# Kernel tuning notes

Hardware: AMD Instinct MI355X
Metric: run time of the kernel (lower is better)

The kernel has to match this reference:

```python
import jax, jax.numpy as jnp
import numpy as np

BIT = 64
N_CLASS = 100
NUM_TRAIN = 100000
BATCH = 512
MU = 1.0   # config['mu']
M = 1.0    # config['m']
ETA = 0.5  # config['eta']
VUL = 1.0  # config['vul']
NTA = 1.0  # config['nta']


def setup_inputs() -> dict:
    key = jax.random.key(0)
    k1, k2, k3, k4, k5, k6 = jax.random.split(key, 6)
    u = jax.random.normal(k1, (BATCH, BIT), jnp.float32)
    # y / Y are one-hot label matrices in DFH; build realistic one-hot floats
    labels = jax.random.randint(k2, (BATCH,), 0, N_CLASS)
    y = jax.nn.one_hot(labels, N_CLASS, dtype=jnp.float32)
    ind = jax.random.randint(k3, (BATCH,), 0, NUM_TRAIN)
    U = jax.random.normal(k4, (BIT, NUM_TRAIN), jnp.float32)
    train_labels = jax.random.randint(k5, (NUM_TRAIN,), 0, N_CLASS)
    Y = jax.nn.one_hot(train_labels, N_CLASS, dtype=jnp.float32).T  # [n_class, num_train]
    V = jax.random.normal(k6, (BIT, N_CLASS), jnp.float32)
    return {"u": u, "y": y, "ind": ind, "U": U, "Y": Y, "V": V}


def _center_gradient(V, y, b):
    # 200-step gradient descent on V minimizing intra + vul*inter + nta*quant.
    n_class = V.shape[1]
    TK = V.shape[0] * (2.0 * jnp.eye(n_class, dtype=V.dtype)
                       - jnp.ones((n_class, n_class), V.dtype))
    yt = y.T  # [n_class, batch]

    def inner_loss(Vc):
        intra = jnp.mean((Vc @ yt - b) ** 2)
        inter = jnp.mean((Vc.T @ Vc - TK) ** 2)
        quant = jnp.mean((Vc - jnp.sign(Vc)) ** 2)
        return intra + VUL * inter + NTA * quant

    grad_fn = jax.grad(inner_loss)

    def step(Vc, i):
        # torch code multiplies alpha by 0.1 *before* the update at i==149 and i==179
        alpha = 0.03 * jnp.where(i >= 149, 0.1, 1.0) * jnp.where(i >= 179, 0.1, 1.0)
        return Vc - alpha * grad_fn(Vc), None

    V_new, _ = jax.lax.scan(step, V, jnp.arange(200))
    return V_new


def reference(u, y, ind, U, Y, V):
    # state buffer updates (torch: self.U[:, ind] = u.t().data, etc.)
    U = U.at[:, ind].set(u.T)
    Y = Y.at[:, ind].set(y.T)
    C = jnp.sign(V)
    b = jnp.sign(MU * (C @ y.T) + u.T)                     # [bit, batch]
    V_new = _center_gradient(V, y, b)                      # updated self.V
    s = (y @ Y > 0).astype(u.dtype)                        # [batch, num_train]
    ip = jnp.clip(0.5 * (u @ U), -100.0, 50.0)             # [batch, num_train]
    metric_loss = jnp.mean((1.0 - s) * jnp.log1p(jnp.exp(M + ip))
                           + s * jnp.log1p(jnp.exp(M - ip)))
    quantization_loss = jnp.mean((b - u.T) ** 2)
    loss = metric_loss + ETA * quantization_loss
    return loss, V_new
```

## Files before the change

kernel.cpp:

```cpp
#include <hip/hip_runtime.h>

#define BIT 64
#define NCLASS 100
#define NTRAIN 100000
#define BATCH 512

#define O_OWNER   0
#define O_LAB     200000
#define O_BSUM    233280
#define O_COUNT   239680
#define O_QSUM    239780
#define O_MSUM    239782

typedef __attribute__((ext_vector_type(8))) short short8v;
typedef __attribute__((ext_vector_type(4))) float f32x4;
typedef unsigned short ushortT;

__device__ __forceinline__ float signf(float x) {
    return (x > 0.f) ? 1.f : ((x < 0.f) ? -1.f : 0.f);
}

__device__ __forceinline__ unsigned cvtpk(float lo, float hi) {
    unsigned r;
    asm("v_cvt_pk_bf16_f32 %0, %1, %2" : "=v"(r) : "v"(lo), "v"(hi));
    return r;
}
__device__ __forceinline__ float dpp_x1(float x) {
    union { float f; int i; } v; v.f = x;
    v.i = __builtin_amdgcn_mov_dpp(v.i, 0xB1, 0xF, 0xF, false);
    return v.f;
}
__device__ __forceinline__ float dpp_x2(float x) {
    union { float f; int i; } v; v.f = x;
    v.i = __builtin_amdgcn_mov_dpp(v.i, 0x4E, 0xF, 0xF, false);
    return v.f;
}

__global__ __launch_bounds__(512) void k_pre(
        const float* __restrict__ y, const int* __restrict__ ind,
        const float* __restrict__ u, const float* __restrict__ V,
        int* owner, int* lab, float* Bsum, float* count, double* qsum) {
    __shared__ float srow[BATCH];
    __shared__ int   labl[BATCH];
    __shared__ double wq[8];
    const int r = blockIdx.x;
    const int bb = threadIdx.x;

    const float* yrow = y + bb * NCLASS;
    int best = 0;
    for (int c = 0; c < NCLASS; ++c)
        if (yrow[c] > 0.5f) best = c;
    labl[bb] = best;
    if (r == 0) {
        lab[bb] = best;
        atomicMax(&owner[ind[bb]], bb);
    }

    const float v  = V[r * NCLASS + best];
    const float uu = u[bb * BIT + r];
    const float bv = signf(signf(v) + uu);
    srow[bb] = bv;
    const float d = bv - uu;
    double q = (double)(d * d);
    for (int off = 32; off; off >>= 1) q += __shfl_down(q, off);
    const int wid = bb >> 6, lane = bb & 63;
    if (lane == 0) wq[wid] = q;
    __syncthreads();
    if (bb == 0) {
        double s = 0;
        for (int w = 0; w < 8; ++w) s += wq[w];
        atomicAdd(qsum, s);
    }

    if (bb < NCLASS) {
        float s = 0.f; int n = 0;
        for (int k = 0; k < BATCH; ++k) {
            const bool hit = (labl[k] == bb);
            s += hit ? srow[k] : 0.f;
            n += hit;
        }
        Bsum[r * NCLASS + bb] = s;
        if (r == 0) count[bb] = (float)n;
    }
}

__global__ __launch_bounds__(512, 4) void k_main(
        const float* __restrict__ V, const float* __restrict__ Bsum,
        const float* __restrict__ count, const float* __restrict__ u,
        const float* __restrict__ U, const float* __restrict__ Y,
        const int* __restrict__ lab, const int* __restrict__ owner,
        double* msum, float* __restrict__ out) {
    __shared__ __align__(16) char smem[69888];

    if (blockIdx.x == 0) {
        ushortT* SAb = (ushortT*)smem;
        ushortT* SBb = (ushortT*)(smem + 32768);
        ushortT* SMf = (ushortT*)(smem + 61440);
        float*   rs  = (float*)(smem + 69632);

        const int t = threadIdx.x, l = t & 63, w = t >> 6;
        const int g = l >> 4, c16 = l & 15;
        const int h = w >> 2;
        const int mtile = w & 3;
        const int m = mtile * 16 + c16;
        const bool dg = ((mtile >> 1) == h);
        const short8v ONES = {0x3F80,0x3F80,0x3F80,0x3F80,
                              0x3F80,0x3F80,0x3F80,0x3F80};

        for (int i = t; i < 16384; i += 512) SAb[i] = 0;
        for (int i = t; i < 14336; i += 512) SBb[i] = 0;

        const float ci = 2.0f / 32768.0f;
        const float ce = 4.0f / 10000.0f;
        const float cq = 2.0f / 6400.0f;
        const float ce64 = 64.0f * ce;

        bool live[4];
        int sbO[4];
        float vreg[4][4], Kc[4][4], ncib[4][4];
        #pragma unroll
        for (int q = 0; q < 4; ++q) {
            const int nt = 4 * h + q;
            const int n0 = nt * 16 + 4 * g;
            const bool wact = (nt < 7);
            live[q] = wact && (n0 < NCLASS);
            sbO[q] = ((nt * 2 + (mtile >> 1)) * 64 +
                      (16 * (c16 >> 2) + 4 * g + (c16 & 3))) * 8 + 4 * (mtile & 1);
            #pragma unroll
            for (int r = 0; r < 4; ++r) {
                float v = 0.f, bs = 0.f, cn = 0.f;
                if (live[q]) {
                    const int n = n0 + r;
                    v  = V[m * NCLASS + n];
                    bs = Bsum[m * NCLASS + n];
                    cn = count[n];
                }
                vreg[q][r] = v;
                Kc[q][r]   = ci * cn + cq - 128.f * ce;
                ncib[q][r] = -ci * bs;
            }
        }
        const int saO0 = (mtile * 4 + 2 * h) * 512 + l * 8;
        const int saO1 = saO0 + 512;

        auto store_frags = [&](ushortT* SAn, ushortT* SBn) {
            uint4 wa;
            wa.x = cvtpk(vreg[0][0], vreg[0][1]);
            wa.y = cvtpk(vreg[0][2], vreg[0][3]);
            wa.z = cvtpk(vreg[1][0], vreg[1][1]);
            wa.w = cvtpk(vreg[1][2], vreg[1][3]);
            *(uint4*)&SAn[saO0] = wa;
            wa.x = cvtpk(vreg[2][0], vreg[2][1]);
            wa.y = cvtpk(vreg[2][2], vreg[2][3]);
            wa.z = cvtpk(vreg[3][0], vreg[3][1]);
            wa.w = cvtpk(vreg[3][2], vreg[3][3]);
            *(uint4*)&SAn[saO1] = wa;
            #pragma unroll
            for (int q = 0; q < 4; ++q) {
                if (4 * h + q < 7) {
                    float a0 = vreg[q][0], a1 = vreg[q][1];
                    float a2 = vreg[q][2], a3 = vreg[q][3];
                    float t0 = dpp_x1(a1), t1 = dpp_x1(a0);
                    float t2 = dpp_x1(a3), t3 = dpp_x1(a2);
                    const bool o1 = (l & 1);
                    float c0 = o1 ? t0 : a0;
                    float c1 = o1 ? a1 : t1;
                    float c2 = o1 ? t2 : a2;
                    float c3 = o1 ? a3 : t3;
                    float u0 = dpp_x2(c2), u1 = dpp_x2(c3);
                    float u2 = dpp_x2(c0), u3 = dpp_x2(c1);
                    const bool o2 = (l & 2);
                    float d0 = o2 ? u0 : c0;
                    float d1 = o2 ? u1 : c1;
                    float d2 = o2 ? c2 : u2;
                    float d3 = o2 ? c3 : u3;
                    uint2 wb;
                    wb.x = cvtpk(d0, d1);
                    wb.y = cvtpk(d2, d3);
                    *(uint2*)&SBn[sbO[q]] = wb;
                }
            }
        };

        __syncthreads();
        store_frags(SAb, SBb);
        __syncthreads();

        int cur = 0;
        for (int step = 0; step < 200; ++step) {
            float alpha = 0.03f;
            if (step >= 149) alpha *= 0.1f;
            if (step >= 179) alpha *= 0.1f;

            const ushortT* SAc = SAb + cur * 8192;

            f32x4 aM0 = {0.f,0.f,0.f,0.f}, aM1 = {0.f,0.f,0.f,0.f};
            f32x4 aR  = {0.f,0.f,0.f,0.f};
            #pragma unroll
            for (int ks = 0; ks < 4; ++ks) {
                short8v b  = *(const short8v*)&SAc[mtile * 2048 + ks * 512 + l * 8];
                short8v a0 = *(const short8v*)&SAc[(2 * h) * 2048 + ks * 512 + l * 8];
                short8v a1 = *(const short8v*)&SAc[(2 * h + 1) * 2048 + ks * 512 + l * 8];
                aM0 = __builtin_amdgcn_mfma_f32_16x16x32_bf16(a0, b, aM0, 0, 0, 0);
                aM1 = __builtin_amdgcn_mfma_f32_16x16x32_bf16(a1, b, aM1, 0, 0, 0);
                if (dg)
                    aR = __builtin_amdgcn_mfma_f32_16x16x32_bf16(b, ONES, aR, 0, 0, 0);
            }
            {
                uint4 sm;
                sm.x = cvtpk(aM0[0], aM0[1]);
                sm.y = cvtpk(aM0[2], aM0[3]);
                sm.z = cvtpk(aM1[0], aM1[1]);
                sm.w = cvtpk(aM1[2], aM1[3]);
                *(uint4*)&SMf[(mtile * 2 + h) * 512 + l * 8] = sm;
            }
            if (dg && c16 == 0)
                *(f32x4*)&rs[mtile * 16 + 4 * g] = aR;
            __syncthreads();

            const ushortT* SBc = SBb + cur * 7168;
            f32x4 p[4];
            #pragma unroll
            for (int q = 0; q < 4; ++q) p[q] = (f32x4){0.f,0.f,0.f,0.f};
            #pragma unroll
            for (int kb = 0; kb < 2; ++kb) {
                short8v bP = *(const short8v*)&SMf[(mtile * 2 + kb) * 512 + l * 8];
                #pragma unroll
                for (int q = 0; q < 4; ++q) {
                    if (4 * h + q < 7) {
                        short8v aP = *(const short8v*)
                            &SBc[((4 * h + q) * 2 + kb) * 512 + l * 8];
                        p[q] = __builtin_amdgcn_mfma_f32_16x16x32_bf16(aP, bP, p[q], 0, 0, 0);
                    }
                }
            }
            const float rsm = rs[m];

            #pragma unroll
            for (int q = 0; q < 4; ++q) {
                if (4 * h + q < 7) {
                    #pragma unroll
                    for (int r = 0; r < 4; ++r) {
                        const float v = vreg[q][r];
                        float t1 = __builtin_fmaf(Kc[q][r], v, ncib[q][r]);
                        t1 = __builtin_fmaf(ce,   p[q][r], t1);
                        t1 = __builtin_fmaf(ce64, rsm,     t1);
                        t1 -= __builtin_copysignf(cq, v);
                        float vn = __builtin_fmaf(-alpha, t1, v);
                        vreg[q][r] = live[q] ? vn : 0.f;
                    }
                }
            }
            store_frags(SAb + (cur ^ 1) * 8192, SBb + (cur ^ 1) * 7168);
            __syncthreads();
            cur ^= 1;
        }

        #pragma unroll
        for (int q = 0; q < 4; ++q) {
            if (live[q]) {
                const int n0 = (4 * h + q) * 16 + 4 * g;
                #pragma unroll
                for (int r = 0; r < 4; ++r)
                    out[1 + m * NCLASS + n0 + r] = vreg[q][r];
            }
        }
    } else {
        float*  ut   = (float*)smem;
        int*    slab = (int*)(smem + 34816);
        double* wsum = (double*)(smem + 36864);
        int*    tls  = (int*)(smem + 36928);

        const int t = threadIdx.x;
        const int jj = t & 255;
        const int j = (blockIdx.x - 1) * 256 + jj;
        const int half = t >> 8;
        const bool jok = (j < NTRAIN);
        slab[t] = lab[t];

        if (half == 0) {
            int tl = 0;
            if (jok) {
                for (int c = 0; c < NCLASS; ++c)
                    if (Y[(size_t)c * NTRAIN + j] > 0.5f) tl = c;
                int ow = owner[j];
                if (ow >= 0) tl = lab[ow];
            }
            tls[jj] = tl;
        }
        __syncthreads();
        const int tl = tls[jj];

        const float* colbase = U;
        size_t cstride = NTRAIN;
        if (jok) {
            int ow = owner[j];
            if (ow >= 0) { colbase = u + (size_t)ow * BIT; cstride = 1; }
            else         { colbase = U + j; }
        }

        float lsum = 0.f;
        for (int ch = 0; ch < 4; ++ch) {
            __syncthreads();
            for (int i = t; i < 8192; i += 512) {
                int buf = i >> 12, k = (i >> 6) & 63, r = i & 63;
                ut[buf * 4352 + r * 68 + k] = u[((buf * 4 + ch) * 64 + k) * BIT + r];
            }
            __syncthreads();

            if (jok) {
                const float* myut = ut + half * 4352;
                float acc[64];
                #pragma unroll
                for (int k = 0; k < 64; ++k) acc[k] = 0.f;
                #pragma unroll 2
                for (int r = 0; r < BIT; ++r) {
                    float Uv = colbase[(size_t)r * cstride];
                    const float* urow = &myut[r * 68];
                    #pragma unroll
                    for (int qq = 0; qq < 16; ++qq) {
                        float4 uv = *(const float4*)&urow[qq * 4];
                        acc[4 * qq + 0] += uv.x * Uv;
                        acc[4 * qq + 1] += uv.y * Uv;
                        acc[4 * qq + 2] += uv.z * Uv;
                        acc[4 * qq + 3] += uv.w * Uv;
                    }
                }
                const int b0 = (half * 4 + ch) * 64;
                #pragma unroll
                for (int k = 0; k < 64; ++k) {
                    float ip = fminf(fmaxf(0.5f * acc[k], -100.f), 50.f);
                    float x = (slab[b0 + k] == tl) ? (1.0f - ip) : (1.0f + ip);
                    lsum += fmaxf(x, 0.f) + __logf(1.f + __expf(-fabsf(x)));
                }
            }
        }

        double d = (double)lsum;
        for (int off = 32; off; off >>= 1) d += __shfl_down(d, off);
        const int wid = t >> 6, lane = t & 63;
        if (lane == 0) wsum[wid] = d;
        __syncthreads();
        if (t == 0) {
            double s = 0;
            for (int ww = 0; ww < 8; ++ww) s += wsum[ww];
            atomicAdd(msum, s);
        }
    }
}

__global__ void k_final(const double* __restrict__ msum,
                        const double* __restrict__ qsum, float* out) {
    if (threadIdx.x == 0) {
        double loss = (*msum) / ((double)BATCH * (double)NTRAIN)
                    + 0.5 * ((*qsum) / ((double)BIT * (double)BATCH));
        out[0] = (float)loss;
    }
}

extern "C" void kernel_launch(void* const* d_in, const int* in_sizes, int n_in,
                              void* d_out, int out_size, void* d_ws, size_t ws_size,
                              hipStream_t stream) {
    const float* u   = (const float*)d_in[0];
    const float* y   = (const float*)d_in[1];
    const int*   ind = (const int*)d_in[2];
    const float* U   = (const float*)d_in[3];
    const float* Y   = (const float*)d_in[4];
    const float* V   = (const float*)d_in[5];
    float* out = (float*)d_out;

    int*   wsI = (int*)d_ws;
    float* wsF = (float*)d_ws;
    int*   owner = wsI + O_OWNER;
    int*   lab   = wsI + O_LAB;
    float* Bsum  = wsF + O_BSUM;
    float* count = wsF + O_COUNT;
    double* qsum = (double*)(wsF + O_QSUM);
    double* msum = (double*)(wsF + O_MSUM);

    hipMemsetAsync(owner, 0xFF, NTRAIN * sizeof(int), stream);
    hipMemsetAsync(wsF + O_QSUM, 0, 4 * sizeof(float), stream);

    k_pre<<<64, 512, 0, stream>>>(y, ind, u, V, owner, lab, Bsum, count, qsum);
    k_main<<<1 + (NTRAIN + 255) / 256, 512, 0, stream>>>(
        V, Bsum, count, u, U, Y, lab, owner, msum, out);
    k_final<<<1, 64, 0, stream>>>(msum, qsum, out);
}
```

Baseline: 364.6 us.

## Precompute transposed u in global memory and split main kernel into noinline bodies

```diff
diff --git a/kernel.cpp b/kernel.cpp
--- a/kernel.cpp
+++ b/kernel.cpp
@@ -7,6 +7,7 @@
 
 #define O_OWNER   0
 #define O_LAB     200000
+#define O_UT      200512
 #define O_BSUM    233280
 #define O_COUNT   239680
 #define O_QSUM    239780
@@ -39,7 +40,8 @@
 __global__ __launch_bounds__(512) void k_pre(
         const float* __restrict__ y, const int* __restrict__ ind,
         const float* __restrict__ u, const float* __restrict__ V,
-        int* owner, int* lab, float* Bsum, float* count, double* qsum) {
+        int* owner, int* lab, float* Bsum, float* count, double* qsum,
+        float* uT) {
     __shared__ float srow[BATCH];
     __shared__ int   labl[BATCH];
     __shared__ double wq[8];
@@ -58,6 +60,7 @@
 
     const float v  = V[r * NCLASS + best];
     const float uu = u[bb * BIT + r];
+    uT[r * BATCH + bb] = uu;
     const float bv = signf(signf(v) + uu);
     srow[bb] = bv;
     const float d = bv - uu;
@@ -84,268 +87,274 @@
     }
 }
 
-__global__ __launch_bounds__(512, 4) void k_main(
+__device__ __noinline__ void gd_body(
+        const float* __restrict__ V, const float* __restrict__ Bsum,
+        const float* __restrict__ count, float* __restrict__ out) {
+    __shared__ ushortT SAb[16384];
+    __shared__ ushortT SBb[14336];
+    __shared__ ushortT SMf[4096];
+    __shared__ float   rs[64];
+    __shared__ float   xpad[4096];
+
+    const int t = threadIdx.x, l = t & 63, w = t >> 6;
+    ((volatile float*)xpad)[t] = 0.f;
+
+    const int g = l >> 4, c16 = l & 15;
+    const int h = w >> 2;
+    const int mtile = w & 3;
+    const int m = mtile * 16 + c16;
+    const bool dg = ((mtile >> 1) == h);
+    const short8v ONES = {0x3F80,0x3F80,0x3F80,0x3F80,
+                          0x3F80,0x3F80,0x3F80,0x3F80};
+
+    for (int i = t; i < 16384; i += 512) SAb[i] = 0;
+    for (int i = t; i < 14336; i += 512) SBb[i] = 0;
+
+    const float ci = 2.0f / 32768.0f;
+    const float ce = 4.0f / 10000.0f;
+    const float cq = 2.0f / 6400.0f;
+    const float ce64 = 64.0f * ce;
+
+    bool live[4];
+    int sbO[4];
+    float vreg[4][4], Kc[4][4], ncib[4][4];
+    #pragma unroll
+    for (int q = 0; q < 4; ++q) {
+        const int nt = 4 * h + q;
+        const int n0 = nt * 16 + 4 * g;
+        const bool wact = (nt < 7);
+        live[q] = wact && (n0 < NCLASS);
+        sbO[q] = ((nt * 2 + (mtile >> 1)) * 64 +
+                  (16 * (c16 >> 2) + 4 * g + (c16 & 3))) * 8 + 4 * (mtile & 1);
+        #pragma unroll
+        for (int r = 0; r < 4; ++r) {
+            float v = 0.f, bs = 0.f, cn = 0.f;
+            if (live[q]) {
+                const int n = n0 + r;
+                v  = V[m * NCLASS + n];
+                bs = Bsum[m * NCLASS + n];
+                cn = count[n];
+            }
+            vreg[q][r] = v;
+            Kc[q][r]   = ci * cn + cq - 128.f * ce;
+            ncib[q][r] = -ci * bs;
+        }
+    }
+    const int saO0 = (mtile * 4 + 2 * h) * 512 + l * 8;
+    const int saO1 = saO0 + 512;
+
+    auto store_frags = [&](ushortT* SAn, ushortT* SBn) {
+        uint4 wa;
+        wa.x = cvtpk(vreg[0][0], vreg[0][1]);
+        wa.y = cvtpk(vreg[0][2], vreg[0][3]);
+        wa.z = cvtpk(vreg[1][0], vreg[1][1]);
+        wa.w = cvtpk(vreg[1][2], vreg[1][3]);
+        *(uint4*)&SAn[saO0] = wa;
+        wa.x = cvtpk(vreg[2][0], vreg[2][1]);
+        wa.y = cvtpk(vreg[2][2], vreg[2][3]);
+        wa.z = cvtpk(vreg[3][0], vreg[3][1]);
+        wa.w = cvtpk(vreg[3][2], vreg[3][3]);
+        *(uint4*)&SAn[saO1] = wa;
+        #pragma unroll
+        for (int q = 0; q < 4; ++q) {
+            if (4 * h + q < 7) {
+                float a0 = vreg[q][0], a1 = vreg[q][1];
+                float a2 = vreg[q][2], a3 = vreg[q][3];
+                float t0 = dpp_x1(a1), t1 = dpp_x1(a0);
+                float t2 = dpp_x1(a3), t3 = dpp_x1(a2);
+                const bool o1 = (l & 1);
+                float c0 = o1 ? t0 : a0;
+                float c1 = o1 ? a1 : t1;
+                float c2 = o1 ? t2 : a2;
+                float c3 = o1 ? a3 : t3;
+                float u0 = dpp_x2(c2), u1 = dpp_x2(c3);
+                float u2 = dpp_x2(c0), u3 = dpp_x2(c1);
+                const bool o2 = (l & 2);
+                float d0 = o2 ? u0 : c0;
+                float d1 = o2 ? u1 : c1;
+                float d2 = o2 ? c2 : u2;
+                float d3 = o2 ? c3 : u3;
+                uint2 wb;
+                wb.x = cvtpk(d0, d1);
+                wb.y = cvtpk(d2, d3);
+                *(uint2*)&SBn[sbO[q]] = wb;
+            }
+        }
+    };
+
+    __syncthreads();
+    store_frags(SAb, SBb);
+    __syncthreads();
+
+    int cur = 0;
+    for (int step = 0; step < 200; ++step) {
+        float alpha = 0.03f;
+        if (step >= 149) alpha *= 0.1f;
+        if (step >= 179) alpha *= 0.1f;
+
+        const ushortT* SAc = SAb + cur * 8192;
+
+        f32x4 aM0 = {0.f,0.f,0.f,0.f}, aM1 = {0.f,0.f,0.f,0.f};
+        f32x4 aR  = {0.f,0.f,0.f,0.f};
+        #pragma unroll
+        for (int ks = 0; ks < 4; ++ks) {
+            short8v b  = *(const short8v*)&SAc[mtile * 2048 + ks * 512 + l * 8];
+            short8v a0 = *(const short8v*)&SAc[(2 * h) * 2048 + ks * 512 + l * 8];
+            short8v a1 = *(const short8v*)&SAc[(2 * h + 1) * 2048 + ks * 512 + l * 8];
+            aM0 = __builtin_amdgcn_mfma_f32_16x16x32_bf16(a0, b, aM0, 0, 0, 0);
+            aM1 = __builtin_amdgcn_mfma_f32_16x16x32_bf16(a1, b, aM1, 0, 0, 0);
+            if (dg)
+                aR = __builtin_amdgcn_mfma_f32_16x16x32_bf16(b, ONES, aR, 0, 0, 0);
+        }
+        {
+            uint4 sm;
+            sm.x = cvtpk(aM0[0], aM0[1]);
+            sm.y = cvtpk(aM0[2], aM0[3]);
+            sm.z = cvtpk(aM1[0], aM1[1]);
+            sm.w = cvtpk(aM1[2], aM1[3]);
+            *(uint4*)&SMf[(mtile * 2 + h) * 512 + l * 8] = sm;
+        }
+        if (dg && c16 == 0)
+            *(f32x4*)&rs[mtile * 16 + 4 * g] = aR;
+        __syncthreads();
+
+        const ushortT* SBc = SBb + cur * 7168;
+        f32x4 p[4];
+        #pragma unroll
+        for (int q = 0; q < 4; ++q) p[q] = (f32x4){0.f,0.f,0.f,0.f};
+        #pragma unroll
+        for (int kb = 0; kb < 2; ++kb) {
+            short8v bP = *(const short8v*)&SMf[(mtile * 2 + kb) * 512 + l * 8];
+            #pragma unroll
+            for (int q = 0; q < 4; ++q) {
+                if (4 * h + q < 7) {
+                    short8v aP = *(const short8v*)
+                        &SBc[((4 * h + q) * 2 + kb) * 512 + l * 8];
+                    p[q] = __builtin_amdgcn_mfma_f32_16x16x32_bf16(aP, bP, p[q], 0, 0, 0);
+                }
+            }
+        }
+        const float rsm = rs[m];
+
+        #pragma unroll
+        for (int q = 0; q < 4; ++q) {
+            if (4 * h + q < 7) {
+                #pragma unroll
+                for (int r = 0; r < 4; ++r) {
+                    const float v = vreg[q][r];
+                    float t1 = __builtin_fmaf(Kc[q][r], v, ncib[q][r]);
+                    t1 = __builtin_fmaf(ce,   p[q][r], t1);
+                    t1 = __builtin_fmaf(ce64, rsm,     t1);
+                    t1 -= __builtin_copysignf(cq, v);
+                    float vn = __builtin_fmaf(-alpha, t1, v);
+                    vreg[q][r] = live[q] ? vn : 0.f;
+                }
+            }
+        }
+        store_frags(SAb + (cur ^ 1) * 8192, SBb + (cur ^ 1) * 7168);
+        __syncthreads();
+        cur ^= 1;
+    }
+
+    #pragma unroll
+    for (int q = 0; q < 4; ++q) {
+        if (live[q]) {
+            const int n0 = (4 * h + q) * 16 + 4 * g;
+            #pragma unroll
+            for (int r = 0; r < 4; ++r)
+                out[1 + m * NCLASS + n0 + r] = vreg[q][r];
+        }
+    }
+}
+
+__device__ __noinline__ void metric_body(
+        const float* __restrict__ u, const float* __restrict__ U,
+        const float* __restrict__ Y, const int* __restrict__ lab,
+        const int* __restrict__ owner, const float* __restrict__ uT,
+        double* msum) {
+    __shared__ double wsumM[8];
+    __shared__ int    tlsM[256];
+
+    const int t = threadIdx.x;
+    const int jj = t & 255;
+    const int j = (blockIdx.x - 1) * 256 + jj;
+    const int half = t >> 8;
+    const bool jok = (j < NTRAIN);
+
+    if (half == 0) {
+        int tl = 0;
+        if (jok) {
+            for (int c = 0; c < NCLASS; ++c)
+                if (Y[(size_t)c * NTRAIN + j] > 0.5f) tl = c;
+            int ow = owner[j];
+            if (ow >= 0) tl = lab[ow];
+        }
+        tlsM[jj] = tl;
+    }
+    __syncthreads();
+    const int tl = tlsM[jj];
+
+    const float* colbase = U;
+    size_t cstride = NTRAIN;
+    if (jok) {
+        int ow = owner[j];
+        if (ow >= 0) { colbase = u + (size_t)ow * BIT; cstride = 1; }
+        else         { colbase = U + j; }
+    }
+
+    float lsum = 0.f;
+    for (int ch = 0; ch < 4; ++ch) {
+        const int b0u = __builtin_amdgcn_readfirstlane((half * 4 + ch) * 64);
+
+        if (jok) {
+            float acc[64];
+            #pragma unroll
+            for (int k = 0; k < 64; ++k) acc[k] = 0.f;
+            #pragma unroll 4
+            for (int r = 0; r < BIT; ++r) {
+                float Uv = colbase[(size_t)r * cstride];
+                const float* urow = &uT[r * BATCH + b0u];
+                #pragma unroll
+                for (int qq = 0; qq < 16; ++qq) {
+                    float4 uv = *(const float4*)&urow[qq * 4];
+                    acc[4 * qq + 0] += uv.x * Uv;
+                    acc[4 * qq + 1] += uv.y * Uv;
+                    acc[4 * qq + 2] += uv.z * Uv;
+                    acc[4 * qq + 3] += uv.w * Uv;
+                }
+            }
+            #pragma unroll
+            for (int k = 0; k < 64; ++k) {
+                const int lv = lab[b0u + k];
+                float ip = fminf(fmaxf(0.5f * acc[k], -100.f), 50.f);
+                float x = (lv == tl) ? (1.0f - ip) : (1.0f + ip);
+                lsum += fmaxf(x, 0.f) + __logf(1.f + __expf(-fabsf(x)));
+            }
+        }
+    }
+
+    double d = (double)lsum;
+    for (int off = 32; off; off >>= 1) d += __shfl_down(d, off);
+    const int wid = t >> 6, lane = t & 63;
+    if (lane == 0) wsumM[wid] = d;
+    __syncthreads();
+    if (t == 0) {
+        double s = 0;
+        for (int ww = 0; ww < 8; ++ww) s += wsumM[ww];
+        atomicAdd(msum, s);
+    }
+}
+
+__global__ __launch_bounds__(512, 2) void k_main(
         const float* __restrict__ V, const float* __restrict__ Bsum,
         const float* __restrict__ count, const float* __restrict__ u,
         const float* __restrict__ U, const float* __restrict__ Y,
         const int* __restrict__ lab, const int* __restrict__ owner,
-        double* msum, float* __restrict__ out) {
-    __shared__ __align__(16) char smem[69888];
-
+        const float* __restrict__ uT, double* msum, float* __restrict__ out) {
     if (blockIdx.x == 0) {
-        ushortT* SAb = (ushortT*)smem;
-        ushortT* SBb = (ushortT*)(smem + 32768);
-        ushortT* SMf = (ushortT*)(smem + 61440);
-        float*   rs  = (float*)(smem + 69632);
-
-        const int t = threadIdx.x, l = t & 63, w = t >> 6;
-        const int g = l >> 4, c16 = l & 15;
-        const int h = w >> 2;
-        const int mtile = w & 3;
-        const int m = mtile * 16 + c16;
-        const bool dg = ((mtile >> 1) == h);
-        const short8v ONES = {0x3F80,0x3F80,0x3F80,0x3F80,
-                              0x3F80,0x3F80,0x3F80,0x3F80};
-
-        for (int i = t; i < 16384; i += 512) SAb[i] = 0;
-        for (int i = t; i < 14336; i += 512) SBb[i] = 0;
-
-        const float ci = 2.0f / 32768.0f;
-        const float ce = 4.0f / 10000.0f;
-        const float cq = 2.0f / 6400.0f;
-        const float ce64 = 64.0f * ce;
-
-        bool live[4];
-        int sbO[4];
-        float vreg[4][4], Kc[4][4], ncib[4][4];
-        #pragma unroll
-        for (int q = 0; q < 4; ++q) {
-            const int nt = 4 * h + q;
-            const int n0 = nt * 16 + 4 * g;
-            const bool wact = (nt < 7);
-            live[q] = wact && (n0 < NCLASS);
-            sbO[q] = ((nt * 2 + (mtile >> 1)) * 64 +
-                      (16 * (c16 >> 2) + 4 * g + (c16 & 3))) * 8 + 4 * (mtile & 1);
-            #pragma unroll
-            for (int r = 0; r < 4; ++r) {
-                float v = 0.f, bs = 0.f, cn = 0.f;
-                if (live[q]) {
-                    const int n = n0 + r;
-                    v  = V[m * NCLASS + n];
-                    bs = Bsum[m * NCLASS + n];
-                    cn = count[n];
-                }
-                vreg[q][r] = v;
-                Kc[q][r]   = ci * cn + cq - 128.f * ce;
-                ncib[q][r] = -ci * bs;
-            }
-        }
-        const int saO0 = (mtile * 4 + 2 * h) * 512 + l * 8;
-        const int saO1 = saO0 + 512;
-
-        auto store_frags = [&](ushortT* SAn, ushortT* SBn) {
-            uint4 wa;
-            wa.x = cvtpk(vreg[0][0], vreg[0][1]);
-            wa.y = cvtpk(vreg[0][2], vreg[0][3]);
-            wa.z = cvtpk(vreg[1][0], vreg[1][1]);
-            wa.w = cvtpk(vreg[1][2], vreg[1][3]);
-            *(uint4*)&SAn[saO0] = wa;
-            wa.x = cvtpk(vreg[2][0], vreg[2][1]);
-            wa.y = cvtpk(vreg[2][2], vreg[2][3]);
-            wa.z = cvtpk(vreg[3][0], vreg[3][1]);
-            wa.w = cvtpk(vreg[3][2], vreg[3][3]);
-            *(uint4*)&SAn[saO1] = wa;
-            #pragma unroll
-            for (int q = 0; q < 4; ++q) {
-                if (4 * h + q < 7) {
-                    float a0 = vreg[q][0], a1 = vreg[q][1];
-                    float a2 = vreg[q][2], a3 = vreg[q][3];
-                    float t0 = dpp_x1(a1), t1 = dpp_x1(a0);
-                    float t2 = dpp_x1(a3), t3 = dpp_x1(a2);
-                    const bool o1 = (l & 1);
-                    float c0 = o1 ? t0 : a0;
-                    float c1 = o1 ? a1 : t1;
-                    float c2 = o1 ? t2 : a2;
-                    float c3 = o1 ? a3 : t3;
-                    float u0 = dpp_x2(c2), u1 = dpp_x2(c3);
-                    float u2 = dpp_x2(c0), u3 = dpp_x2(c1);
-                    const bool o2 = (l & 2);
-                    float d0 = o2 ? u0 : c0;
-                    float d1 = o2 ? u1 : c1;
-                    float d2 = o2 ? c2 : u2;
-                    float d3 = o2 ? c3 : u3;
-                    uint2 wb;
-                    wb.x = cvtpk(d0, d1);
-                    wb.y = cvtpk(d2, d3);
-                    *(uint2*)&SBn[sbO[q]] = wb;
-                }
-            }
-        };
-
-        __syncthreads();
-        store_frags(SAb, SBb);
-        __syncthreads();
-
-        int cur = 0;
-        for (int step = 0; step < 200; ++step) {
-            float alpha = 0.03f;
-            if (step >= 149) alpha *= 0.1f;
-            if (step >= 179) alpha *= 0.1f;
-
-            const ushortT* SAc = SAb + cur * 8192;
-
-            f32x4 aM0 = {0.f,0.f,0.f,0.f}, aM1 = {0.f,0.f,0.f,0.f};
-            f32x4 aR  = {0.f,0.f,0.f,0.f};
-            #pragma unroll
-            for (int ks = 0; ks < 4; ++ks) {
-                short8v b  = *(const short8v*)&SAc[mtile * 2048 + ks * 512 + l * 8];
-                short8v a0 = *(const short8v*)&SAc[(2 * h) * 2048 + ks * 512 + l * 8];
-                short8v a1 = *(const short8v*)&SAc[(2 * h + 1) * 2048 + ks * 512 + l * 8];
-                aM0 = __builtin_amdgcn_mfma_f32_16x16x32_bf16(a0, b, aM0, 0, 0, 0);
-                aM1 = __builtin_amdgcn_mfma_f32_16x16x32_bf16(a1, b, aM1, 0, 0, 0);
-                if (dg)
-                    aR = __builtin_amdgcn_mfma_f32_16x16x32_bf16(b, ONES, aR, 0, 0, 0);
-            }
-            {
-                uint4 sm;
-                sm.x = cvtpk(aM0[0], aM0[1]);
-                sm.y = cvtpk(aM0[2], aM0[3]);
-                sm.z = cvtpk(aM1[0], aM1[1]);
-                sm.w = cvtpk(aM1[2], aM1[3]);
-                *(uint4*)&SMf[(mtile * 2 + h) * 512 + l * 8] = sm;
-            }
-            if (dg && c16 == 0)
-                *(f32x4*)&rs[mtile * 16 + 4 * g] = aR;
-            __syncthreads();
-
-            const ushortT* SBc = SBb + cur * 7168;
-            f32x4 p[4];
-            #pragma unroll
-            for (int q = 0; q < 4; ++q) p[q] = (f32x4){0.f,0.f,0.f,0.f};
-            #pragma unroll
-            for (int kb = 0; kb < 2; ++kb) {
-                short8v bP = *(const short8v*)&SMf[(mtile * 2 + kb) * 512 + l * 8];
-                #pragma unroll
-                for (int q = 0; q < 4; ++q) {
-                    if (4 * h + q < 7) {
-                        short8v aP = *(const short8v*)
-                            &SBc[((4 * h + q) * 2 + kb) * 512 + l * 8];
-                        p[q] = __builtin_amdgcn_mfma_f32_16x16x32_bf16(aP, bP, p[q], 0, 0, 0);
-                    }
-                }
-            }
-            const float rsm = rs[m];
-
-            #pragma unroll
-            for (int q = 0; q < 4; ++q) {
-                if (4 * h + q < 7) {
-                    #pragma unroll
-                    for (int r = 0; r < 4; ++r) {
-                        const float v = vreg[q][r];
-                        float t1 = __builtin_fmaf(Kc[q][r], v, ncib[q][r]);
-                        t1 = __builtin_fmaf(ce,   p[q][r], t1);
-                        t1 = __builtin_fmaf(ce64, rsm,     t1);
-                        t1 -= __builtin_copysignf(cq, v);
-                        float vn = __builtin_fmaf(-alpha, t1, v);
-                        vreg[q][r] = live[q] ? vn : 0.f;
-                    }
-                }
-            }
-            store_frags(SAb + (cur ^ 1) * 8192, SBb + (cur ^ 1) * 7168);
-            __syncthreads();
-            cur ^= 1;
-        }
-
-        #pragma unroll
-        for (int q = 0; q < 4; ++q) {
-            if (live[q]) {
-                const int n0 = (4 * h + q) * 16 + 4 * g;
-                #pragma unroll
-                for (int r = 0; r < 4; ++r)
-                    out[1 + m * NCLASS + n0 + r] = vreg[q][r];
-            }
-        }
+        gd_body(V, Bsum, count, out);
     } else {
-        float*  ut   = (float*)smem;
-        int*    slab = (int*)(smem + 34816);
-        double* wsum = (double*)(smem + 36864);
-        int*    tls  = (int*)(smem + 36928);
-
-        const int t = threadIdx.x;
-        const int jj = t & 255;
-        const int j = (blockIdx.x - 1) * 256 + jj;
-        const int half = t >> 8;
-        const bool jok = (j < NTRAIN);
-        slab[t] = lab[t];
-
-        if (half == 0) {
-            int tl = 0;
-            if (jok) {
-                for (int c = 0; c < NCLASS; ++c)
-                    if (Y[(size_t)c * NTRAIN + j] > 0.5f) tl = c;
-                int ow = owner[j];
-                if (ow >= 0) tl = lab[ow];
-            }
-            tls[jj] = tl;
-        }
-        __syncthreads();
-        const int tl = tls[jj];
-
-        const float* colbase = U;
-        size_t cstride = NTRAIN;
-        if (jok) {
-            int ow = owner[j];
-            if (ow >= 0) { colbase = u + (size_t)ow * BIT; cstride = 1; }
-            else         { colbase = U + j; }
-        }
-
-        float lsum = 0.f;
-        for (int ch = 0; ch < 4; ++ch) {
-            __syncthreads();
-            for (int i = t; i < 8192; i += 512) {
-                int buf = i >> 12, k = (i >> 6) & 63, r = i & 63;
-                ut[buf * 4352 + r * 68 + k] = u[((buf * 4 + ch) * 64 + k) * BIT + r];
-            }
-            __syncthreads();
-
-            if (jok) {
-                const float* myut = ut + half * 4352;
-                float acc[64];
-                #pragma unroll
-                for (int k = 0; k < 64; ++k) acc[k] = 0.f;
-                #pragma unroll 2
-                for (int r = 0; r < BIT; ++r) {
-                    float Uv = colbase[(size_t)r * cstride];
-                    const float* urow = &myut[r * 68];
-                    #pragma unroll
-                    for (int qq = 0; qq < 16; ++qq) {
-                        float4 uv = *(const float4*)&urow[qq * 4];
-                        acc[4 * qq + 0] += uv.x * Uv;
-                        acc[4 * qq + 1] += uv.y * Uv;
-                        acc[4 * qq + 2] += uv.z * Uv;
-                        acc[4 * qq + 3] += uv.w * Uv;
-                    }
-                }
-                const int b0 = (half * 4 + ch) * 64;
-                #pragma unroll
-                for (int k = 0; k < 64; ++k) {
-                    float ip = fminf(fmaxf(0.5f * acc[k], -100.f), 50.f);
-                    float x = (slab[b0 + k] == tl) ? (1.0f - ip) : (1.0f + ip);
-                    lsum += fmaxf(x, 0.f) + __logf(1.f + __expf(-fabsf(x)));
-                }
-            }
-        }
-
-        double d = (double)lsum;
-        for (int off = 32; off; off >>= 1) d += __shfl_down(d, off);
-        const int wid = t >> 6, lane = t & 63;
-        if (lane == 0) wsum[wid] = d;
-        __syncthreads();
-        if (t == 0) {
-            double s = 0;
-            for (int ww = 0; ww < 8; ++ww) s += wsum[ww];
-            atomicAdd(msum, s);
-        }
+        metric_body(u, U, Y, lab, owner, uT, msum);
     }
 }
 
@@ -373,6 +382,7 @@
     float* wsF = (float*)d_ws;
     int*   owner = wsI + O_OWNER;
     int*   lab   = wsI + O_LAB;
+    float* uT    = wsF + O_UT;
     float* Bsum  = wsF + O_BSUM;
     float* count = wsF + O_COUNT;
     double* qsum = (double*)(wsF + O_QSUM);
@@ -381,8 +391,8 @@
     hipMemsetAsync(owner, 0xFF, NTRAIN * sizeof(int), stream);
     hipMemsetAsync(wsF + O_QSUM, 0, 4 * sizeof(float), stream);
 
-    k_pre<<<64, 512, 0, stream>>>(y, ind, u, V, owner, lab, Bsum, count, qsum);
+    k_pre<<<64, 512, 0, stream>>>(y, ind, u, V, owner, lab, Bsum, count, qsum, uT);
     k_main<<<1 + (NTRAIN + 255) / 256, 512, 0, stream>>>(
-        V, Bsum, count, u, U, Y, lab, owner, msum, out);
+        V, Bsum, count, u, U, Y, lab, owner, uT, msum, out);
     k_final<<<1, 64, 0, stream>>>(msum, qsum, out);
 }
```

New measurement: 756.5 us. 2.07x slower.
